# Kernel tuning notes

Hardware: AMD Instinct MI355X
Metric: run time of the kernel (lower is better)

## Reference

```python
import jax, jax.numpy as jnp
import numpy as np

DIM = 1024
HEADS = 16
DIM_HEAD = 64
INNER = HEADS * DIM_HEAD  # 1024
MLP = 4096
EPS = 1e-5


def layer_norm(x, gamma, beta):
    mu = jnp.mean(x, axis=-1, keepdims=True)
    var = jnp.var(x, axis=-1, keepdims=True)
    return (x - mu) * jax.lax.rsqrt(var + EPS) * gamma + beta


def setup_inputs() -> dict:
    key = jax.random.key(0)
    ks = jax.random.split(key, 10)
    s = 0.02
    return {
        "x": jax.random.normal(ks[0], (2, 2048, DIM), dtype=jnp.float32),
        "ln1_g": jnp.ones((DIM,), jnp.float32),
        "ln1_b": jnp.zeros((DIM,), jnp.float32),
        "w_qkv": jax.random.normal(ks[1], (DIM, 3 * INNER), jnp.float32) * s,
        "w_out": jax.random.normal(ks[2], (INNER, DIM), jnp.float32) * s,
        "b_out": jnp.zeros((DIM,), jnp.float32),
        "ln2_g": jnp.ones((DIM,), jnp.float32),
        "ln2_b": jnp.zeros((DIM,), jnp.float32),
        "w1": jax.random.normal(ks[3], (DIM, MLP), jnp.float32) * s,
        "b1": jnp.zeros((MLP,), jnp.float32),
        "w2": jax.random.normal(ks[4], (MLP, DIM), jnp.float32) * s,
        "b2": jnp.zeros((DIM,), jnp.float32),
    }


def reference(x, ln1_g, ln1_b, w_qkv, w_out, b_out, ln2_g, ln2_b, w1, b1, w2, b2):
    b, n, _ = x.shape
    scale = DIM_HEAD ** -0.5

    # --- attention sublayer (pre-norm) ---
    h = layer_norm(x, ln1_g, ln1_b)
    qkv = h @ w_qkv  # [b, n, 3*inner]
    q, k, v = jnp.split(qkv, 3, axis=-1)
    # [b, n, inner] -> [b, heads, n, dim_head]
    def to_heads(t):
        return t.reshape(b, n, HEADS, DIM_HEAD).transpose(0, 2, 1, 3)
    q, k, v = to_heads(q), to_heads(k), to_heads(v)
    dots = jnp.einsum('bhid,bhjd->bhij', q, k) * scale  # [b,h,n,n]
    attn = jax.nn.softmax(dots, axis=-1)
    out = jnp.einsum('bhij,bhjd->bhid', attn, v)
    out = out.transpose(0, 2, 1, 3).reshape(b, n, INNER)
    x = out @ w_out + b_out + x

    # --- FFN sublayer (pre-norm) ---
    h = layer_norm(x, ln2_g, ln2_b)
    h = jax.nn.gelu(h @ w1 + b1, approximate=False)
    x = h @ w2 + b2 + x
    return x
```

## Files before the change

### kernel.cpp

```cpp
#include <hip/hip_runtime.h>
#include <hip/hip_bf16.h>
#include <math.h>

#define SEQ 2048
#define BATCH 2
#define TOKENS 4096
#define HEADS 16
#define DHEAD 64
#define TOKSTRIDE 3072

typedef __attribute__((ext_vector_type(4))) float f32x4;
typedef __attribute__((ext_vector_type(16))) float f32x16;
typedef __attribute__((ext_vector_type(8))) __bf16 bf16x8;
typedef __attribute__((ext_vector_type(8))) unsigned short ushort8;
typedef __attribute__((ext_vector_type(4))) unsigned short ushort4_t;
typedef __attribute__((ext_vector_type(4))) unsigned u32x4;
typedef __attribute__((ext_vector_type(2))) unsigned u32x2;

#if __has_builtin(__builtin_amdgcn_exp2f)
#define EXP2(x) __builtin_amdgcn_exp2f(x)
#else
#define EXP2(x) exp2f(x)
#endif

#if __has_builtin(__builtin_amdgcn_permlane32_swap)
#define HAS_PL32 1
#else
#define HAS_PL32 0
#endif

__device__ __forceinline__ unsigned short f2bf(float f) {
  unsigned u = __builtin_bit_cast(unsigned, f);
  u += 0x7fffu + ((u >> 16) & 1u);
  return (unsigned short)(u >> 16);
}

__device__ __forceinline__ float bf2f(unsigned short s) {
  unsigned u = ((unsigned)s) << 16;
  return __builtin_bit_cast(float, u);
}

__device__ __forceinline__ unsigned cvt_pk_bf16(float lo, float hi) {
  unsigned r;
  asm("v_cvt_pk_bf16_f32 %0, %1, %2" : "=v"(r) : "v"(lo), "v"(hi));
  return r;
}

__device__ __forceinline__ void cp16(const void* g, void* l) {
  __builtin_amdgcn_global_load_lds((const __attribute__((address_space(1))) void*)g,
                                   (__attribute__((address_space(3))) void*)l, 16, 0, 0);
}

#define FENCE asm volatile("" ::: "memory")
#define BARR  do { FENCE; __builtin_amdgcn_s_barrier(); FENCE; } while (0)

__global__ __launch_bounds__(256) void ln_rows(const float* __restrict__ x,
                                               const float* __restrict__ g,
                                               const float* __restrict__ b,
                                               unsigned short* __restrict__ out) {
  const int row = blockIdx.x;
  const int t = threadIdx.x;
  const f32x4* x4 = (const f32x4*)(x + (size_t)row * 1024);
  f32x4 v = x4[t];
  float sum = v[0] + v[1] + v[2] + v[3];
  float ss  = v[0]*v[0] + v[1]*v[1] + v[2]*v[2] + v[3]*v[3];
#pragma unroll
  for (int off = 1; off < 64; off <<= 1) {
    sum += __shfl_xor(sum, off);
    ss  += __shfl_xor(ss, off);
  }
  __shared__ float red[8];
  const int w = t >> 6, l = t & 63;
  if (l == 0) { red[w] = sum; red[w + 4] = ss; }
  __syncthreads();
  sum = red[0] + red[1] + red[2] + red[3];
  ss  = red[4] + red[5] + red[6] + red[7];
  const float mean = sum * (1.0f / 1024.0f);
  const float var  = ss * (1.0f / 1024.0f) - mean * mean;
  const float rs = rsqrtf(var + 1e-5f);
  ushort4_t o;
#pragma unroll
  for (int j = 0; j < 4; ++j) {
    float gv = g[t * 4 + j], bv = b[t * 4 + j];
    o[j] = f2bf((v[j] - mean) * rs * gv + bv);
  }
  *(ushort4_t*)(out + (size_t)row * 1024 + t * 4) = o;
}

__global__ __launch_bounds__(256) void ln_rows_bf(const unsigned short* __restrict__ x,
                                                  const float* __restrict__ g,
                                                  const float* __restrict__ b,
                                                  unsigned short* __restrict__ out) {
  const int row = blockIdx.x;
  const int t = threadIdx.x;
  ushort4_t v4 = *(const ushort4_t*)(x + (size_t)row * 1024 + t * 4);
  float v[4] = {bf2f(v4[0]), bf2f(v4[1]), bf2f(v4[2]), bf2f(v4[3])};
  float sum = v[0] + v[1] + v[2] + v[3];
  float ss  = v[0]*v[0] + v[1]*v[1] + v[2]*v[2] + v[3]*v[3];
#pragma unroll
  for (int off = 1; off < 64; off <<= 1) {
    sum += __shfl_xor(sum, off);
    ss  += __shfl_xor(ss, off);
  }
  __shared__ float red[8];
  const int w = t >> 6, l = t & 63;
  if (l == 0) { red[w] = sum; red[w + 4] = ss; }
  __syncthreads();
  sum = red[0] + red[1] + red[2] + red[3];
  ss  = red[4] + red[5] + red[6] + red[7];
  const float mean = sum * (1.0f / 1024.0f);
  const float var  = ss * (1.0f / 1024.0f) - mean * mean;
  const float rs = rsqrtf(var + 1e-5f);
  ushort4_t o;
#pragma unroll
  for (int j = 0; j < 4; ++j) {
    float gv = g[t * 4 + j], bv = b[t * 4 + j];
    o[j] = f2bf((v[j] - mean) * rs * gv + bv);
  }
  *(ushort4_t*)(out + (size_t)row * 1024 + t * 4) = o;
}

__global__ __launch_bounds__(256) void transpose_cast(const float* __restrict__ w,
                                                      unsigned short* __restrict__ wt,
                                                      int K, int N, float scale, int nscaled) {
  __shared__ float tile[32][33];
  const int n0 = blockIdx.x * 32, k0 = blockIdx.y * 32;
  const int tx = threadIdx.x & 31;
  const int ty = threadIdx.x >> 5;
#pragma unroll
  for (int i = 0; i < 4; ++i)
    tile[ty + 8 * i][tx] = w[(size_t)(k0 + ty + 8 * i) * N + n0 + tx];
  __syncthreads();
#pragma unroll
  for (int i = 0; i < 4; ++i) {
    int n = n0 + ty + 8 * i;
    float s = (n < nscaled) ? scale : 1.0f;
    wt[(size_t)n * K + k0 + tx] = f2bf(tile[tx][ty + 8 * i] * s);
  }
}

template <int EPI, int BN, int MINW, int NSPLIT>
__global__ __launch_bounds__(256, MINW) void gemm_bt(
    const unsigned short* __restrict__ A, const unsigned short* __restrict__ Bt,
    void* __restrict__ Cp, const float* __restrict__ bias, const void* __restrict__ resv,
    int M, int N, int K) {
  constexpr int BM = 128, BK = 64;
  constexpr int MR = BM / 32, NR = BN / 32;
  constexpr int AIT = BM * BK / 2048;
  constexpr int BIT = BN * BK / 2048;
  __shared__ unsigned short la[BM * BK];
  __shared__ unsigned short lb[BN * BK];
  const int t = threadIdx.x;
  const int w = t >> 6, l = t & 63;
  const int nwg = gridDim.x;
  const int bid = blockIdx.x;
  const int bid2 = (bid & 7) * (nwg >> 3) + (bid >> 3);
  const int nmn = nwg / NSPLIT;
  const int ksl = bid2 / nmn;
  const int rmn = bid2 - ksl * nmn;
  const int nx = N / BN;
  const int m0 = (rmn / nx) * BM, n0 = (rmn % nx) * BN;
  const int klen = K / NSPLIT;
  const int kbeg = ksl * klen;
  const int wr = w >> 1, wc = w & 1;
  const int lrow = l & 15, lk4 = l >> 4;
  f32x4 acc[MR][NR] = {};

  for (int k0 = kbeg; k0 < kbeg + klen; k0 += BK) {
#pragma unroll
    for (int i = 0; i < AIT; ++i) {
      int idx = t + 256 * i;
      int row = idx >> 3, seg = idx & 7;
      int ss = seg ^ (row & 7);
      cp16(A + (size_t)(m0 + row) * K + k0 + ss * 8, (char*)la + w * 1024 + i * 4096);
    }
#pragma unroll
    for (int i = 0; i < BIT; ++i) {
      int idx = t + 256 * i;
      int row = idx >> 3, seg = idx & 7;
      int ss = seg ^ (row & 7);
      cp16(Bt + (size_t)(n0 + row) * K + k0 + ss * 8, (char*)lb + w * 1024 + i * 4096);
    }
    __syncthreads();
#pragma unroll
    for (int ks = 0; ks < 2; ++ks) {
      bf16x8 af[MR], bfr[NR];
#pragma unroll
      for (int mi = 0; mi < MR; ++mi) {
        int row = wr * (BM / 2) + mi * 16 + lrow;
        int ss = (ks * 4 + lk4) ^ (row & 7);
        af[mi] = *(const bf16x8*)((const char*)la + row * 128 + ss * 16);
      }
#pragma unroll
      for (int ni = 0; ni < NR; ++ni) {
        int row = wc * (BN / 2) + ni * 16 + lrow;
        int ss = (ks * 4 + lk4) ^ (row & 7);
        bfr[ni] = *(const bf16x8*)((const char*)lb + row * 128 + ss * 16);
      }
#pragma unroll
      for (int mi = 0; mi < MR; ++mi)
#pragma unroll
        for (int ni = 0; ni < NR; ++ni)
          acc[mi][ni] = __builtin_amdgcn_mfma_f32_16x16x32_bf16(af[mi], bfr[ni], acc[mi][ni], 0, 0, 0);
    }
    __syncthreads();
  }

#pragma unroll
  for (int mi = 0; mi < MR; ++mi) {
    int rowb = m0 + wr * (BM / 2) + mi * 16 + lk4 * 4;
#pragma unroll
    for (int ni = 0; ni < NR; ++ni) {
      int col = n0 + wc * (BN / 2) + ni * 16 + lrow;
      f32x4 a = acc[mi][ni];
#pragma unroll
      for (int r = 0; r < 4; ++r) {
        size_t off = (size_t)(rowb + r) * N + col;
        if (EPI == 0) {
          ((unsigned short*)Cp)[off] = f2bf(a[r]);
        } else if (EPI == 2) {
          float v = a[r] + bias[col];
          ((unsigned short*)Cp)[off] = f2bf(0.5f * v * (1.0f + erff(v * 0.70710678f)));
        } else if (EPI == 3) {
          ((unsigned short*)Cp)[off] = f2bf(a[r] + bias[col] + ((const float*)resv)[off]);
        } else if (EPI == 4) {
          ((float*)Cp)[off] = a[r] + bias[col] + bf2f(((const unsigned short*)resv)[off]);
        } else {
          ((float*)Cp)[(size_t)ksl * M * N + off] = a[r];
        }
      }
    }
  }
}

__global__ __launch_bounds__(256) void mlp2_combine(const float* __restrict__ p,
                                                    const float* __restrict__ b2,
                                                    const unsigned short* __restrict__ xa,
                                                    float* __restrict__ out) {
  const int row = blockIdx.x, t = threadIdx.x;
  const size_t off = (size_t)row * 1024 + t * 4;
  f32x4 a = *(const f32x4*)(p + off);
  f32x4 b = *(const f32x4*)(p + (size_t)TOKENS * 1024 + off);
  f32x4 bb = *(const f32x4*)(b2 + t * 4);
  ushort4_t xv = *(const ushort4_t*)(xa + off);
  f32x4 o;
#pragma unroll
  for (int j = 0; j < 4; ++j) o[j] = a[j] + b[j] + bb[j] + bf2f(xv[j]);
  *(f32x4*)(out + off) = o;
}

__global__ __launch_bounds__(256, 2) void attn4(const unsigned short* __restrict__ qkv,
                                                unsigned short* __restrict__ Op,
                                                float2* __restrict__ ml) {
  __shared__ unsigned short lk_[64 * 64];
  __shared__ unsigned short lvt[64 * 64];
  const int t = threadIdx.x, wv = t >> 6, l = t & 63;
  const int chunk = blockIdx.x & 3, qb = blockIdx.x >> 2;
  const int h = blockIdx.y, b = blockIdx.z;
  const size_t tok0 = (size_t)b * SEQ;
  const int lq = l & 31, hi = l >> 5, l7 = l & 7;
  const int qrow = qb * 128 + wv * 32 + lq;
  const int kstart = chunk * 8;

  bf16x8 qf[4];
#pragma unroll
  for (int dc = 0; dc < 4; ++dc)
    qf[dc] = *(const bf16x8*)(qkv + (tok0 + qrow) * TOKSTRIDE + h * DHEAD + dc * 16 + hi * 8);

  float mrun = -1e30f, lsum = 0.0f;
  f32x16 o0 = {}, o1 = {};

  {
#pragma unroll
    for (int i = 0; i < 2; ++i) {
      int idx = t + 256 * i;
      int key = idx >> 3, seg = idx & 7;
      cp16(qkv + (tok0 + kstart * 64 + key) * TOKSTRIDE + 1024 + h * DHEAD + ((seg ^ (key & 7)) << 3),
           (char*)lk_ + wv * 1024 + i * 4096);
    }
#pragma unroll
    for (int i = 0; i < 2; ++i) {
      int idx = t + 256 * i;
      int key = idx & 63, seg = idx >> 6;
      ushort8 v8 = *(const ushort8*)(qkv + (tok0 + kstart * 64 + key) * TOKSTRIDE + 2048 + h * DHEAD + seg * 8);
#pragma unroll
      for (int j = 0; j < 8; ++j) {
        int d = seg * 8 + j;
        lvt[d * 64 + (((key >> 3) ^ (d & 7)) << 3) + (key & 7)] = v8[j];
      }
    }
  }
  __syncthreads();

  for (int kb = 0; kb < 8; ++kb) {
    const bool more = (kb + 1 < 8);
    const int kpre = kstart + kb + 1;

    f32x16 s0 = {}, s1 = {};
    __builtin_amdgcn_s_setprio(1);
#pragma unroll
    for (int dc = 0; dc < 4; ++dc) {
      int sgA = (dc * 2 + hi) ^ l7;
      bf16x8 kf0 = *(const bf16x8*)((const char*)lk_ + lq * 128 + (sgA << 4));
      bf16x8 kf1 = *(const bf16x8*)((const char*)lk_ + (32 + lq) * 128 + (sgA << 4));
      s0 = __builtin_amdgcn_mfma_f32_32x32x16_bf16(kf0, qf[dc], s0, 0, 0, 0);
      s1 = __builtin_amdgcn_mfma_f32_32x32x16_bf16(kf1, qf[dc], s1, 0, 0, 0);
    }
    __builtin_amdgcn_s_setprio(0);

    asm volatile("s_waitcnt lgkmcnt(0)" ::: "memory");
    BARR;
    __builtin_amdgcn_sched_barrier(0);

    ushort8 vpre[2];
    if (more) {
#pragma unroll
      for (int i = 0; i < 2; ++i) {
        int idx = t + 256 * i;
        int key = idx >> 3, seg = idx & 7;
        cp16(qkv + (tok0 + kpre * 64 + key) * TOKSTRIDE + 1024 + h * DHEAD + ((seg ^ (key & 7)) << 3),
             (char*)lk_ + wv * 1024 + i * 4096);
      }
#pragma unroll
      for (int i = 0; i < 2; ++i) {
        int idx = t + 256 * i;
        int key = idx & 63, seg = idx >> 6;
        vpre[i] = *(const ushort8*)(qkv + (tok0 + kpre * 64 + key) * TOKSTRIDE + 2048 + h * DHEAD + seg * 8);
      }
    }

    float mx[8];
#pragma unroll
    for (int r = 0; r < 8; ++r)
      mx[r] = fmaxf(fmaxf(s0[r], s0[r + 8]), fmaxf(s1[r], s1[r + 8]));
#pragma unroll
    for (int r = 0; r < 4; ++r) mx[r] = fmaxf(mx[r], mx[r + 4]);
    float m01 = fmaxf(fmaxf(mx[0], mx[1]), fmaxf(mx[2], mx[3]));
    float pm = fmaxf(m01, __shfl_xor(m01, 32));

    if (__any(pm > mrun + 8.0f)) {
      float mn = fmaxf(mrun, pm);
      float alpha = EXP2(mrun - mn);
      mrun = mn;
      lsum *= alpha;
#pragma unroll
      for (int r = 0; r < 16; ++r) {
        int qi = (r & 3) + 8 * (r >> 2) + 4 * hi;
        float ar = __shfl(alpha, qi);
        o0[r] *= ar; o1[r] *= ar;
      }
    }

    float p0[16], p1[16], ts[16];
#pragma unroll
    for (int r = 0; r < 16; ++r) { p0[r] = EXP2(s0[r] - mrun); }
#pragma unroll
    for (int r = 0; r < 16; ++r) { p1[r] = EXP2(s1[r] - mrun); }
#pragma unroll
    for (int r = 0; r < 16; ++r) ts[r] = p0[r] + p1[r];
#pragma unroll
    for (int st = 8; st > 0; st >>= 1)
#pragma unroll
      for (int r = 0; r < 8; ++r)
        if (r < st) ts[r] += ts[r + st];
    float psum = ts[0] + __shfl_xor(ts[0], 32);
    lsum += psum;

    unsigned W0[8], W1[8];
#pragma unroll
    for (int mI = 0; mI < 8; ++mI) {
      W0[mI] = cvt_pk_bf16(p0[2 * mI], p0[2 * mI + 1]);
      W1[mI] = cvt_pk_bf16(p1[2 * mI], p1[2 * mI + 1]);
    }
#if !HAS_PL32
    unsigned X0[8], X1[8];
#pragma unroll
    for (int mI = 0; mI < 8; ++mI) {
      X0[mI] = __shfl_xor((int)W0[mI], 32);
      X1[mI] = __shfl_xor((int)W1[mI], 32);
    }
#endif

    __builtin_amdgcn_s_setprio(1);
#pragma unroll
    for (int kt = 0; kt < 2; ++kt) {
#pragma unroll
      for (int c = 0; c < 2; ++c) {
        u32x4 fw;
#if HAS_PL32
        unsigned a0 = (kt == 0) ? W0[4 * c + 0] : W1[4 * c + 0];
        unsigned a1 = (kt == 0) ? W0[4 * c + 1] : W1[4 * c + 1];
        unsigned b0 = (kt == 0) ? W0[4 * c + 2] : W1[4 * c + 2];
        unsigned b1 = (kt == 0) ? W0[4 * c + 3] : W1[4 * c + 3];
        u32x2 pa = __builtin_amdgcn_permlane32_swap(a0, b0, false, false);
        u32x2 pb = __builtin_amdgcn_permlane32_swap(a1, b1, false, false);
        fw[0] = pa[0]; fw[1] = pb[0]; fw[2] = pa[1]; fw[3] = pb[1];
#else
        if (kt == 0) {
          fw[0] = hi ? X0[4 * c + 2] : W0[4 * c + 0];
          fw[1] = hi ? X0[4 * c + 3] : W0[4 * c + 1];
          fw[2] = hi ? W0[4 * c + 2] : X0[4 * c + 0];
          fw[3] = hi ? W0[4 * c + 3] : X0[4 * c + 1];
        } else {
          fw[0] = hi ? X1[4 * c + 2] : W1[4 * c + 0];
          fw[1] = hi ? X1[4 * c + 3] : W1[4 * c + 1];
          fw[2] = hi ? W1[4 * c + 2] : X1[4 * c + 0];
          fw[3] = hi ? W1[4 * c + 3] : X1[4 * c + 1];
        }
#endif
        bf16x8 pf = __builtin_bit_cast(bf16x8, fw);
        int ksg = (kt * 4 + c * 2 + hi) ^ l7;
        bf16x8 vfA = *(const bf16x8*)((const char*)lvt + lq * 128 + (ksg << 4));
        bf16x8 vfB = *(const bf16x8*)((const char*)lvt + (32 + lq) * 128 + (ksg << 4));
        o0 = __builtin_amdgcn_mfma_f32_32x32x16_bf16(pf, vfA, o0, 0, 0, 0);
        o1 = __builtin_amdgcn_mfma_f32_32x32x16_bf16(pf, vfB, o1, 0, 0, 0);
      }
    }
    __builtin_amdgcn_s_setprio(0);

    asm volatile("s_waitcnt lgkmcnt(0)" ::: "memory");
    BARR;
    __builtin_amdgcn_sched_barrier(0);

    if (more) {
#pragma unroll
      for (int i = 0; i < 2; ++i) {
        int idx = t + 256 * i;
        int key = idx & 63, seg = idx >> 6;
#pragma unroll
        for (int j = 0; j < 8; ++j) {
          int d = seg * 8 + j;
          lvt[d * 64 + (((key >> 3) ^ (d & 7)) << 3) + (key & 7)] = vpre[i][j];
        }
      }
    }
    asm volatile("s_waitcnt vmcnt(0) lgkmcnt(0)" ::: "memory");
    BARR;
    __builtin_amdgcn_sched_barrier(0);
  }

  const size_t cbase = (size_t)chunk * TOKENS;
#pragma unroll
  for (int r = 0; r < 16; ++r) {
    int qi = (r & 3) + 8 * (r >> 2) + 4 * hi;
    size_t rowoff = (cbase + tok0 + qb * 128 + wv * 32 + qi) * (size_t)1024 + h * DHEAD;
    Op[rowoff + lq]      = f2bf(o0[r]);
    Op[rowoff + 32 + lq] = f2bf(o1[r]);
  }
  if (l < 32) {
    size_t tokr = tok0 + qb * 128 + wv * 32 + lq;
    ml[(cbase + tokr) * 16 + h] = make_float2(mrun, lsum);
  }
}

__global__ __launch_bounds__(256) void attn_combine4(const unsigned short* __restrict__ Op,
                                                     const float2* __restrict__ ml,
                                                     unsigned short* __restrict__ out) {
  const int t = threadIdx.x, w = t >> 6, l = t & 63;
  const size_t tok = blockIdx.x * 4 + w;
#pragma unroll
  for (int h = 0; h < 16; ++h) {
    float2 mm[4];
#pragma unroll
    for (int c = 0; c < 4; ++c) mm[c] = ml[((size_t)c * TOKENS + tok) * 16 + h];
    float M = fmaxf(fmaxf(mm[0].x, mm[1].x), fmaxf(mm[2].x, mm[3].x));
    float wgt[4];
    float den = 0.0f;
#pragma unroll
    for (int c = 0; c < 4; ++c) { wgt[c] = EXP2(mm[c].x - M); den += mm[c].y * wgt[c]; }
    float inv = 1.0f / den;
    int col = h * 64 + l;
    float o = 0.0f;
#pragma unroll
    for (int c = 0; c < 4; ++c)
      o += bf2f(Op[((size_t)c * TOKENS + tok) * 1024 + col]) * wgt[c];
    out[tok * 1024 + col] = f2bf(o * inv);
  }
}

extern "C" void kernel_launch(void* const* d_in, const int* in_sizes, int n_in,
                              void* d_out, int out_size, void* d_ws, size_t ws_size,
                              hipStream_t stream) {
  const float* x    = (const float*)d_in[0];
  const float* ln1g = (const float*)d_in[1];
  const float* ln1b = (const float*)d_in[2];
  const float* wqkv = (const float*)d_in[3];
  const float* wout = (const float*)d_in[4];
  const float* bout = (const float*)d_in[5];
  const float* ln2g = (const float*)d_in[6];
  const float* ln2b = (const float*)d_in[7];
  const float* w1   = (const float*)d_in[8];
  const float* b1   = (const float*)d_in[9];
  const float* w2   = (const float*)d_in[10];
  const float* b2   = (const float*)d_in[11];

  char* ws = (char*)d_ws;
  unsigned short* wqkvT = (unsigned short*)ws; ws += (size_t)3072 * 1024 * 2;
  unsigned short* woutT = (unsigned short*)ws; ws += (size_t)1024 * 1024 * 2;
  unsigned short* w1T   = (unsigned short*)ws; ws += (size_t)4096 * 1024 * 2;
  unsigned short* w2T   = (unsigned short*)ws; ws += (size_t)1024 * 4096 * 2;
  unsigned short* h1    = (unsigned short*)ws; ws += (size_t)TOKENS * 1024 * 2;
  unsigned short* qkvb  = (unsigned short*)ws; ws += (size_t)TOKENS * 3072 * 2;
  unsigned short* attno = (unsigned short*)ws; ws += (size_t)TOKENS * 1024 * 2;
  unsigned short* xa    = (unsigned short*)ws; ws += (size_t)TOKENS * 1024 * 4;
  unsigned short* h2    = (unsigned short*)ws; ws += (size_t)TOKENS * 1024 * 2;
  unsigned short* hid   = (unsigned short*)ws; ws += (size_t)TOKENS * 4096 * 2;
  float2*         mlbuf = (float2*)ws;         ws += (size_t)4 * TOKENS * 16 * 8;
  unsigned short* Opart = hid;
  float*          mlp2p = (float*)h1;

  transpose_cast<<<dim3(3072 / 32, 1024 / 32), 256, 0, stream>>>(wqkv, wqkvT, 1024, 3072, 0.18033688f, 1024);
  transpose_cast<<<dim3(1024 / 32, 1024 / 32), 256, 0, stream>>>(wout, woutT, 1024, 1024, 1.0f, 0);
  transpose_cast<<<dim3(4096 / 32, 1024 / 32), 256, 0, stream>>>(w1, w1T, 1024, 4096, 1.0f, 0);
  transpose_cast<<<dim3(1024 / 32, 4096 / 32), 256, 0, stream>>>(w2, w2T, 4096, 1024, 1.0f, 0);

  ln_rows<<<TOKENS, 256, 0, stream>>>(x, ln1g, ln1b, h1);
  gemm_bt<0, 128, 2, 1><<<768, 256, 0, stream>>>(h1, wqkvT, qkvb, nullptr, nullptr, TOKENS, 3072, 1024);
  attn4<<<dim3(4 * SEQ / 128, HEADS, BATCH), 256, 0, stream>>>(qkvb, Opart, mlbuf);
  attn_combine4<<<TOKENS / 4, 256, 0, stream>>>(Opart, mlbuf, attno);
  gemm_bt<3, 64, 3, 1><<<512, 256, 0, stream>>>(attno, woutT, xa, bout, x, TOKENS, 1024, 1024);
  ln_rows_bf<<<TOKENS, 256, 0, stream>>>(xa, ln2g, ln2b, h2);
  gemm_bt<2, 128, 2, 1><<<1024, 256, 0, stream>>>(h2, w1T, hid, b1, nullptr, TOKENS, 4096, 1024);
  gemm_bt<5, 128, 2, 2><<<512, 256, 0, stream>>>(hid, w2T, mlp2p, nullptr, nullptr, TOKENS, 1024, 4096);
  mlp2_combine<<<TOKENS, 256, 0, stream>>>(mlp2p, b2, xa, (float*)d_out);
}
```

Measured before the change: 242.6 us.

## Double-buffer K/V tiles in attention and store MLP2 split-K partials as bf16

The attention kernel now keeps two LDS buffers for K and V. The next tile's loads are issued before computing on the current tile, which cuts the three barriers per key block down to one __syncthreads. Separately, the split-K partial sums of the second MLP GEMM are written as bf16 instead of fp32, halving that intermediate traffic in the combine kernel. The costs are double the LDS use, which may hurt occupancy at two blocks per CU, a redundant reload on the last iteration, and reduced precision in the partial sums.

After: 249.2 us. 2.7% more time.

```diff
diff --git a/kernel.cpp b/kernel.cpp
--- a/kernel.cpp
+++ b/kernel.cpp
@@ -50,9 +50,6 @@
   __builtin_amdgcn_global_load_lds((const __attribute__((address_space(1))) void*)g,
                                    (__attribute__((address_space(3))) void*)l, 16, 0, 0);
 }
-
-#define FENCE asm volatile("" ::: "memory")
-#define BARR  do { FENCE; __builtin_amdgcn_s_barrier(); FENCE; } while (0)
 
 __global__ __launch_bounds__(256) void ln_rows(const float* __restrict__ x,
                                                const float* __restrict__ g,
@@ -226,34 +223,34 @@
         } else if (EPI == 4) {
           ((float*)Cp)[off] = a[r] + bias[col] + bf2f(((const unsigned short*)resv)[off]);
         } else {
-          ((float*)Cp)[(size_t)ksl * M * N + off] = a[r];
+          ((unsigned short*)Cp)[(size_t)ksl * M * N + off] = f2bf(a[r]);
         }
       }
     }
   }
 }
 
-__global__ __launch_bounds__(256) void mlp2_combine(const float* __restrict__ p,
+__global__ __launch_bounds__(256) void mlp2_combine(const unsigned short* __restrict__ p,
                                                     const float* __restrict__ b2,
                                                     const unsigned short* __restrict__ xa,
                                                     float* __restrict__ out) {
   const int row = blockIdx.x, t = threadIdx.x;
   const size_t off = (size_t)row * 1024 + t * 4;
-  f32x4 a = *(const f32x4*)(p + off);
-  f32x4 b = *(const f32x4*)(p + (size_t)TOKENS * 1024 + off);
+  ushort4_t a = *(const ushort4_t*)(p + off);
+  ushort4_t b = *(const ushort4_t*)(p + (size_t)TOKENS * 1024 + off);
   f32x4 bb = *(const f32x4*)(b2 + t * 4);
   ushort4_t xv = *(const ushort4_t*)(xa + off);
   f32x4 o;
 #pragma unroll
-  for (int j = 0; j < 4; ++j) o[j] = a[j] + b[j] + bb[j] + bf2f(xv[j]);
+  for (int j = 0; j < 4; ++j) o[j] = bf2f(a[j]) + bf2f(b[j]) + bb[j] + bf2f(xv[j]);
   *(f32x4*)(out + off) = o;
 }
 
-__global__ __launch_bounds__(256, 2) void attn4(const unsigned short* __restrict__ qkv,
+__global__ __launch_bounds__(256, 2) void attn5(const unsigned short* __restrict__ qkv,
                                                 unsigned short* __restrict__ Op,
                                                 float2* __restrict__ ml) {
-  __shared__ unsigned short lk_[64 * 64];
-  __shared__ unsigned short lvt[64 * 64];
+  __shared__ unsigned short lk_[2][64 * 64];
+  __shared__ unsigned short lvt[2][64 * 64];
   const int t = threadIdx.x, wv = t >> 6, l = t & 63;
   const int chunk = blockIdx.x & 3, qb = blockIdx.x >> 2;
   const int h = blockIdx.y, b = blockIdx.z;
@@ -276,7 +273,7 @@
       int idx = t + 256 * i;
       int key = idx >> 3, seg = idx & 7;
       cp16(qkv + (tok0 + kstart * 64 + key) * TOKSTRIDE + 1024 + h * DHEAD + ((seg ^ (key & 7)) << 3),
-           (char*)lk_ + wv * 1024 + i * 4096);
+           (char*)lk_[0] + wv * 1024 + i * 4096);
     }
 #pragma unroll
     for (int i = 0; i < 2; ++i) {
@@ -286,48 +283,42 @@
 #pragma unroll
       for (int j = 0; j < 8; ++j) {
         int d = seg * 8 + j;
-        lvt[d * 64 + (((key >> 3) ^ (d & 7)) << 3) + (key & 7)] = v8[j];
+        lvt[0][d * 64 + (((key >> 3) ^ (d & 7)) << 3) + (key & 7)] = v8[j];
       }
     }
   }
   __syncthreads();
 
+  int cur = 0;
   for (int kb = 0; kb < 8; ++kb) {
-    const bool more = (kb + 1 < 8);
-    const int kpre = kstart + kb + 1;
+    const int nxt = cur ^ 1;
+    const int kpre = kstart + ((kb + 1 < 8) ? kb + 1 : kb);
+#pragma unroll
+    for (int i = 0; i < 2; ++i) {
+      int idx = t + 256 * i;
+      int key = idx >> 3, seg = idx & 7;
+      cp16(qkv + (tok0 + kpre * 64 + key) * TOKSTRIDE + 1024 + h * DHEAD + ((seg ^ (key & 7)) << 3),
+           (char*)lk_[nxt] + wv * 1024 + i * 4096);
+    }
+    ushort8 vpre[2];
+#pragma unroll
+    for (int i = 0; i < 2; ++i) {
+      int idx = t + 256 * i;
+      int key = idx & 63, seg = idx >> 6;
+      vpre[i] = *(const ushort8*)(qkv + (tok0 + kpre * 64 + key) * TOKSTRIDE + 2048 + h * DHEAD + seg * 8);
+    }
 
     f32x16 s0 = {}, s1 = {};
     __builtin_amdgcn_s_setprio(1);
 #pragma unroll
     for (int dc = 0; dc < 4; ++dc) {
       int sgA = (dc * 2 + hi) ^ l7;
-      bf16x8 kf0 = *(const bf16x8*)((const char*)lk_ + lq * 128 + (sgA << 4));
-      bf16x8 kf1 = *(const bf16x8*)((const char*)lk_ + (32 + lq) * 128 + (sgA << 4));
+      bf16x8 kf0 = *(const bf16x8*)((const char*)lk_[cur] + lq * 128 + (sgA << 4));
+      bf16x8 kf1 = *(const bf16x8*)((const char*)lk_[cur] + (32 + lq) * 128 + (sgA << 4));
       s0 = __builtin_amdgcn_mfma_f32_32x32x16_bf16(kf0, qf[dc], s0, 0, 0, 0);
       s1 = __builtin_amdgcn_mfma_f32_32x32x16_bf16(kf1, qf[dc], s1, 0, 0, 0);
     }
     __builtin_amdgcn_s_setprio(0);
-
-    asm volatile("s_waitcnt lgkmcnt(0)" ::: "memory");
-    BARR;
-    __builtin_amdgcn_sched_barrier(0);
-
-    ushort8 vpre[2];
-    if (more) {
-#pragma unroll
-      for (int i = 0; i < 2; ++i) {
-        int idx = t + 256 * i;
-        int key = idx >> 3, seg = idx & 7;
-        cp16(qkv + (tok0 + kpre * 64 + key) * TOKSTRIDE + 1024 + h * DHEAD + ((seg ^ (key & 7)) << 3),
-             (char*)lk_ + wv * 1024 + i * 4096);
-      }
-#pragma unroll
-      for (int i = 0; i < 2; ++i) {
-        int idx = t + 256 * i;
-        int key = idx & 63, seg = idx >> 6;
-        vpre[i] = *(const ushort8*)(qkv + (tok0 + kpre * 64 + key) * TOKSTRIDE + 2048 + h * DHEAD + seg * 8);
-      }
-    }
 
     float mx[8];
 #pragma unroll
@@ -410,33 +401,26 @@
 #endif
         bf16x8 pf = __builtin_bit_cast(bf16x8, fw);
         int ksg = (kt * 4 + c * 2 + hi) ^ l7;
-        bf16x8 vfA = *(const bf16x8*)((const char*)lvt + lq * 128 + (ksg << 4));
-        bf16x8 vfB = *(const bf16x8*)((const char*)lvt + (32 + lq) * 128 + (ksg << 4));
+        bf16x8 vfA = *(const bf16x8*)((const char*)lvt[cur] + lq * 128 + (ksg << 4));
+        bf16x8 vfB = *(const bf16x8*)((const char*)lvt[cur] + (32 + lq) * 128 + (ksg << 4));
         o0 = __builtin_amdgcn_mfma_f32_32x32x16_bf16(pf, vfA, o0, 0, 0, 0);
         o1 = __builtin_amdgcn_mfma_f32_32x32x16_bf16(pf, vfB, o1, 0, 0, 0);
       }
     }
     __builtin_amdgcn_s_setprio(0);
 
-    asm volatile("s_waitcnt lgkmcnt(0)" ::: "memory");
-    BARR;
-    __builtin_amdgcn_sched_barrier(0);
-
-    if (more) {
-#pragma unroll
-      for (int i = 0; i < 2; ++i) {
-        int idx = t + 256 * i;
-        int key = idx & 63, seg = idx >> 6;
-#pragma unroll
-        for (int j = 0; j < 8; ++j) {
-          int d = seg * 8 + j;
-          lvt[d * 64 + (((key >> 3) ^ (d & 7)) << 3) + (key & 7)] = vpre[i][j];
-        }
-      }
-    }
-    asm volatile("s_waitcnt vmcnt(0) lgkmcnt(0)" ::: "memory");
-    BARR;
-    __builtin_amdgcn_sched_barrier(0);
+#pragma unroll
+    for (int i = 0; i < 2; ++i) {
+      int idx = t + 256 * i;
+      int key = idx & 63, seg = idx >> 6;
+#pragma unroll
+      for (int j = 0; j < 8; ++j) {
+        int d = seg * 8 + j;
+        lvt[nxt][d * 64 + (((key >> 3) ^ (d & 7)) << 3) + (key & 7)] = vpre[i][j];
+      }
+    }
+    __syncthreads();
+    cur = nxt;
   }
 
   const size_t cbase = (size_t)chunk * TOKENS;
@@ -507,7 +491,7 @@
   unsigned short* hid   = (unsigned short*)ws; ws += (size_t)TOKENS * 4096 * 2;
   float2*         mlbuf = (float2*)ws;         ws += (size_t)4 * TOKENS * 16 * 8;
   unsigned short* Opart = hid;
-  float*          mlp2p = (float*)h1;
+  unsigned short* mlp2p = h1;
 
   transpose_cast<<<dim3(3072 / 32, 1024 / 32), 256, 0, stream>>>(wqkv, wqkvT, 1024, 3072, 0.18033688f, 1024);
   transpose_cast<<<dim3(1024 / 32, 1024 / 32), 256, 0, stream>>>(wout, woutT, 1024, 1024, 1.0f, 0);
@@ -516,7 +500,7 @@
 
   ln_rows<<<TOKENS, 256, 0, stream>>>(x, ln1g, ln1b, h1);
   gemm_bt<0, 128, 2, 1><<<768, 256, 0, stream>>>(h1, wqkvT, qkvb, nullptr, nullptr, TOKENS, 3072, 1024);
-  attn4<<<dim3(4 * SEQ / 128, HEADS, BATCH), 256, 0, stream>>>(qkvb, Opart, mlbuf);
+  attn5<<<dim3(4 * SEQ / 128, HEADS, BATCH), 256, 0, stream>>>(qkvb, Opart, mlbuf);
   attn_combine4<<<TOKENS / 4, 256, 0, stream>>>(Opart, mlbuf, attno);
   gemm_bt<3, 64, 3, 1><<<512, 256, 0, stream>>>(attno, woutT, xa, bout, x, TOKENS, 1024, 1024);
   ln_rows_bf<<<TOKENS, 256, 0, stream>>>(xa, ln2g, ln2b, h2);
```
